# Performance work log

Measured on AMD Instinct MI355X. Metric: run time of the kernel, lower is better.

## Reference

```python
import jax, jax.numpy as jnp
import numpy as np

NUM_HEADS = 8
N_WIN = 7
TOPK = 4


def _grid2seq(x, rs, m):
    # x: (B, C, H, W) -> (B, m, nregion, reg_size, head_dim)
    B, C, H, W = x.shape
    rh, rw = H // rs[0], W // rs[1]
    d = C // m
    x = x.reshape(B, m, d, rh, rs[0], rw, rs[1])
    x = jnp.einsum('bmdhpwq->bmhwpqd', x).reshape(B, m, rh * rw, rs[0] * rs[1], d)
    return x, rh, rw


def _seq2grid(x, rh, rw, rs):
    B, m, nreg, rsq, d = x.shape
    x = x.reshape(B, m, rh, rw, rs[0], rs[1], d)
    return jnp.einsum('bmhwpqd->bmdhpwq', x).reshape(B, m * d, rh * rs[0], rw * rs[1])


def setup_inputs() -> dict:
    key = jax.random.key(0)
    ks = jax.random.split(key, 7)
    C = 256
    inp = {
        'x': jax.random.normal(ks[0], (16, C, 56, 56), jnp.float32),
        'w_qkv': jax.random.normal(ks[1], (3 * C, C), jnp.float32) * 0.02,
        'b_qkv': jax.random.normal(ks[2], (3 * C,), jnp.float32) * 0.02,
        'w_lepe': jax.random.normal(ks[3], (C, 1, 3, 3), jnp.float32) * 0.02,
        'b_lepe': jax.random.normal(ks[4], (C,), jnp.float32) * 0.02,
        'w_out': jax.random.normal(ks[5], (C, C), jnp.float32) * 0.02,
        'b_out': jax.random.normal(ks[6], (C,), jnp.float32) * 0.02,
    }
    return inp


def reference(x, w_qkv, b_qkv, w_lepe, b_lepe, w_out, b_out):
    N, C, H, W = x.shape
    m = NUM_HEADS
    d = C // m
    scale = d ** (-0.5)
    rs = (max(1, H // N_WIN), max(1, W // N_WIN))  # (8, 8) here; H,W divisible -> no pad
    rh, rw = H // rs[0], W // rs[1]

    # 1x1 conv qkv projection
    qkv = jnp.einsum('nchw,oc->nohw', x, w_qkv) + b_qkv[None, :, None, None]
    q, k, v = jnp.split(qkv, 3, axis=1)

    # region-level routing (avg_pool over each region; exact divisibility -> plain mean)
    def region_mean(t):
        return t.reshape(N, C, rh, rs[0], rw, rs[1]).mean(axis=(3, 5))  # (N,C,rh,rw)

    q_r = jax.lax.stop_gradient(region_mean(q)).reshape(N, C, rh * rw).transpose(0, 2, 1)  # (N,nreg,C)
    k_r = jax.lax.stop_gradient(region_mean(k)).reshape(N, C, rh * rw)  # (N,C,nreg)
    a_r = q_r @ k_r  # (N, nreg, nreg)
    k_fixed = min(TOPK, a_r.shape[-1])
    _, idx_r = jax.lax.top_k(a_r, k_fixed)  # (N, nreg, topk)
    idx_r = jnp.broadcast_to(idx_r[:, None], (N, m, rh * rw, k_fixed))  # (N,m,nreg,topk)

    # token-level attention within routed regions
    q_seq, _, _ = _grid2seq(q, rs, m)  # (N,m,nreg,rs2,d)
    k_seq, _, _ = _grid2seq(k, rs, m)
    v_seq, _, _ = _grid2seq(v, rs, m)
    rs2 = k_seq.shape[-2]

    gather = jax.vmap(jax.vmap(lambda seq, i: seq[i]))  # over (batch, head)
    key_g = gather(k_seq, idx_r).reshape(N, m, rh * rw, k_fixed * rs2, d)
    val_g = gather(v_seq, idx_r).reshape(N, m, rh * rw, k_fixed * rs2, d)

    attn = jax.nn.softmax(jnp.einsum('bmnpd,bmnkd->bmnpk', q_seq * scale, key_g), axis=-1)
    out = jnp.einsum('bmnpk,bmnkd->bmnpd', attn, val_g)
    out = _seq2grid(out, rh, rw, rs)  # (N, C, H, W)

    # LEPE: depthwise 3x3 conv on v
    lepe = jax.lax.conv_general_dilated(
        v, w_lepe, window_strides=(1, 1), padding='SAME',
        feature_group_count=C, dimension_numbers=('NCHW', 'OIHW', 'NCHW'))
    out = out + lepe + b_lepe[None, :, None, None]

    # 1x1 conv output projection
    out = jnp.einsum('nchw,oc->nohw', out, w_out) + b_out[None, :, None, None]
    return out
```

## Files before the change

### kernel.cpp

```cpp
#include <hip/hip_runtime.h>
#include <cstdint>

#define DEV __device__ __forceinline__

using short8 = __attribute__((ext_vector_type(8))) short;
using f32x4  = __attribute__((ext_vector_type(4))) float;

#define MFMA __builtin_amdgcn_mfma_f32_16x16x32_bf16

DEV float bf2f(unsigned short u){
  union { unsigned int i; float f; } v; v.i = ((unsigned int)u) << 16; return v.f;
}
DEV unsigned short f2bf(float f){
  union { float f; unsigned int i; } v; v.f = f;
  unsigned int x = v.i;
  return (unsigned short)((x + 0x7fffu + ((x >> 16) & 1u)) >> 16);
}
DEV unsigned int cvtpk(float a, float b){
  unsigned int r;
  asm("v_cvt_pk_bf16_f32 %0, %1, %2" : "=v"(r) : "v"(a), "v"(b));
  return r;
}

__global__ __launch_bounds__(256) void k_prep(const float* __restrict__ w_qkv,
                                              const float* __restrict__ w_out,
                                              unsigned short* __restrict__ wqh_t,
                                              unsigned short* __restrict__ woh_t,
                                              unsigned short* __restrict__ wol_t){
  int i = blockIdx.x*256 + threadIdx.x;
  if (i < 196608){
    int o = i >> 8, c = i & 255, kc = c >> 5, kk = c & 31;
    wqh_t[kc*24576 + o*32 + kk] = f2bf(w_qkv[i]);
  } else {
    int j = i - 196608;
    if (j < 65536){
      int o = j >> 8, c = j & 255, kc = c >> 5, kk = c & 31;
      float v = w_out[j];
      unsigned short h = f2bf(v);
      int dst = kc*8192 + o*32 + kk;
      woh_t[dst] = h;
      wol_t[dst] = f2bf(v - bf2f(h));
    }
  }
}

__global__ __launch_bounds__(256) void k_qrkr(const float* __restrict__ xbar,
                                              const float* __restrict__ w_qkv,
                                              const float* __restrict__ b_qkv,
                                              float* __restrict__ q_r,
                                              float* __restrict__ k_r){
  __shared__ float4 xb4[448];
  const int wb = blockIdx.x, n = blockIdx.y, rz = blockIdx.z, t = threadIdx.x;
  {
    const float4* src = (const float4*)(xbar + (size_t)n*12544) + rz*448;
    for (int i = t; i < 448; i += 256) xb4[i] = src[i];
  }
  const int wrow = wb*64 + (t>>2), kl = t&3;
  float4 wreg[16];
  {
    const float4* wsrc = (const float4*)(w_qkv + (size_t)wrow*256) + kl*16;
    #pragma unroll
    for (int i = 0; i < 16; ++i) wreg[i] = wsrc[i];
  }
  __syncthreads();
  const float bias = b_qkv[wrow];
  for (int rl = 0; rl < 7; ++rl){
    float s = 0.f;
    #pragma unroll
    for (int i = 0; i < 16; ++i){
      float4 a = wreg[i], b = xb4[rl*64 + kl*16 + i];
      s += a.x*b.x + a.y*b.y + a.z*b.z + a.w*b.w;
    }
    s += __shfl_xor(s, 1, 64);
    s += __shfl_xor(s, 2, 64);
    if (kl == 0){
      int reg = rz*7 + rl;
      if (wrow < 256) q_r[((size_t)n*49 + reg)*256 + wrow] = s + bias;
      else            k_r[((size_t)n*49 + reg)*256 + wrow - 256] = s + bias;
    }
  }
}

__global__ __launch_bounds__(64) void k_topk(const float* __restrict__ q_r,
                                             const float* __restrict__ k_r,
                                             int* __restrict__ idx){
  __shared__ float sc[49];
  const int qreg = blockIdx.x, n = blockIdx.y, l = threadIdx.x;
  const float* qrow = q_r + ((size_t)n*49 + qreg)*256;
  const float q0 = qrow[l], q1 = qrow[l+64], q2 = qrow[l+128], q3 = qrow[l+192];
  for (int kr = 0; kr < 49; ++kr){
    const float* krow = k_r + ((size_t)n*49 + kr)*256;
    float s = q0*krow[l] + q1*krow[l+64] + q2*krow[l+128] + q3*krow[l+192];
    #pragma unroll
    for (int m = 1; m < 64; m <<= 1) s += __shfl_xor(s, m, 64);
    if (l == 0) sc[kr] = s;
  }
  __syncthreads();
  if (l == 0){
    #pragma unroll
    for (int s = 0; s < 4; ++s){
      float best = -3.4e38f; int bi = 0;
      for (int kr = 0; kr < 49; ++kr) if (sc[kr] > best){ best = sc[kr]; bi = kr; }
      idx[((size_t)n*49 + qreg)*4 + s] = bi;
      sc[bi] = -3.4e38f;
    }
  }
}

__global__ __launch_bounds__(256) void k_qkv(const float* __restrict__ x,
                                             const unsigned short* __restrict__ wqh_t,
                                             const float* __restrict__ b_qkv,
                                             unsigned short* __restrict__ q_rm,
                                             unsigned short* __restrict__ k_rm,
                                             unsigned short* __restrict__ v_t,
                                             float* __restrict__ xbar){
  __shared__ unsigned short xl[64*256];
  const int lin = blockIdx.x;
  const int xcd = lin & 7, jj = lin >> 3;
  const int jobid = xcd*294 + jj;
  const int z = jobid % 3;
  const int pair = jobid / 3;
  const int reg = pair % 49, n = pair / 49;

  const int ry = reg/7, rx = reg%7;
  const int t = threadIdx.x, w = t>>6, g = (t>>4)&3, c16 = t&15;
  {
    const int pq = (t & 15)*4, cc = t >> 4;
    const int row = pq >> 3, col = pq & 7;
    const float* src = x + ((size_t)n*256 + cc)*3136 + (ry*8 + row)*56 + rx*8 + col;
    float rs[16];
    #pragma unroll
    for (int ci = 0; ci < 16; ++ci){
      float4 v4 = *reinterpret_cast<const float4*>(src + (size_t)ci*16*3136);
      int c = ci*16 + cc;
      xl[((pq+0)*256 + c) ^ (((pq+0)&15)<<3)] = f2bf(v4.x);
      xl[((pq+1)*256 + c) ^ (((pq+1)&15)<<3)] = f2bf(v4.y);
      xl[((pq+2)*256 + c) ^ (((pq+2)&15)<<3)] = f2bf(v4.z);
      xl[((pq+3)*256 + c) ^ (((pq+3)&15)<<3)] = f2bf(v4.w);
      rs[ci] = v4.x + v4.y + v4.z + v4.w;
    }
    if (z == 0){
      #pragma unroll
      for (int ci = 0; ci < 16; ++ci){
        float r = rs[ci];
        r += __shfl_xor(r, 1, 64);
        r += __shfl_xor(r, 2, 64);
        r += __shfl_xor(r, 4, 64);
        r += __shfl_xor(r, 8, 64);
        if ((t & 15) == 0)
          xbar[((size_t)n*49 + reg)*256 + ci*16 + (t>>4)] = r * (1.0f/64.0f);
      }
    }
  }
  __syncthreads();
  const size_t rb = (size_t)(n*8)*49 + reg;
  const int osw = w*16;

  if (z < 2){
    f32x4 acc[4][4] = {};
    for (int kc = 0; kc < 8; ++kc){
      short8 xf[4];
      #pragma unroll
      for (int pt = 0; pt < 4; ++pt){
        int p = pt*16 + c16;
        xf[pt] = *reinterpret_cast<const short8*>(&xl[(p*256 + kc*32 + 8*g) ^ ((p&15)<<3)]);
      }
      #pragma unroll
      for (int oi = 0; oi < 4; ++oi){
        const int os = z*256 + oi*64 + osw;
        short8 wf = *reinterpret_cast<const short8*>(wqh_t + (size_t)kc*24576 + (os + c16)*32 + 8*g);
        #pragma unroll
        for (int pt = 0; pt < 4; ++pt)
          acc[oi][pt] = MFMA(xf[pt], wf, acc[oi][pt], 0, 0, 0);
      }
    }
    #pragma unroll
    for (int oi = 0; oi < 4; ++oi){
      const int o = z*256 + oi*64 + osw + c16;
      const float bias = b_qkv[o];
      const int oc = o & 255, hh = oc >> 5, dd = oc & 31;
      unsigned short* dst = ((z == 0) ? q_rm : k_rm) + (rb + hh*49)*2048 + dd;
      #pragma unroll
      for (int pt = 0; pt < 4; ++pt)
        #pragma unroll
        for (int r = 0; r < 4; ++r){
          int tok = pt*16 + 4*g + r;
          dst[tok*32] = f2bf(acc[oi][pt][r] + bias);
        }
    }
  } else {
    f32x4 acc[4][4] = {};
    for (int kc = 0; kc < 8; ++kc){
      short8 xf[4];
      #pragma unroll
      for (int pt = 0; pt < 4; ++pt){
        int p = pt*16 + c16;
        xf[pt] = *reinterpret_cast<const short8*>(&xl[(p*256 + kc*32 + 8*g) ^ ((p&15)<<3)]);
      }
      #pragma unroll
      for (int oi = 0; oi < 4; ++oi){
        const int os = oi*64 + osw;
        short8 wf = *reinterpret_cast<const short8*>(wqh_t + (size_t)kc*24576 + (512 + os + c16)*32 + 8*g);
        #pragma unroll
        for (int pt = 0; pt < 4; ++pt)
          acc[oi][pt] = MFMA(wf, xf[pt], acc[oi][pt], 0, 0, 0);
      }
    }
    #pragma unroll
    for (int oi = 0; oi < 4; ++oi){
      #pragma unroll
      for (int r = 0; r < 4; ++r){
        int c = oi*64 + osw + 4*g + r;
        const float bias = b_qkv[512 + c];
        int hh = c >> 5, ch = c & 31;
        unsigned short* dst = v_t + (rb + hh*49)*2048 + ch*32;
        #pragma unroll
        for (int pt = 0; pt < 4; ++pt){
          int tok = pt*16 + c16;
          dst[(tok>>5)*1024 + (tok&31)] = f2bf(acc[oi][pt][r] + bias);
        }
      }
    }
  }
}

__global__ __launch_bounds__(256, 4) void k_attn(const unsigned short* __restrict__ q_rm,
                                                 const unsigned short* __restrict__ k_rm,
                                                 const unsigned short* __restrict__ v_t,
                                                 const int* __restrict__ idx,
                                                 const float* __restrict__ w_lepe,
                                                 const float* __restrict__ b_lepe,
                                                 unsigned short* __restrict__ att_hi,
                                                 unsigned short* __restrict__ att_lo){
  __shared__ unsigned short halo[10*320];
  __shared__ float wl_s[288];
  __shared__ float bl_s[32];

  const int lin = blockIdx.x + 49*(blockIdx.y + 8*blockIdx.z);
  const int xcd = lin & 7, j = lin >> 3;
  const int jq = j / 49;
  const int qreg = j - jq*49;
  const int hn = jq*8 + xcd;
  const int h = hn & 7, n = hn >> 3;

  const int t = threadIdx.x, w = t>>6, g = (t>>4)&3, c16 = t&15;
  const int ry = qreg/7, rx = qreg%7;
  const int gy0 = ry*8;

  int4 ridx = *reinterpret_cast<const int4*>(idx + ((size_t)n*49 + qreg)*4);
  int regs[4] = {ridx.x, ridx.y, ridx.z, ridx.w};

  const size_t hb = ((size_t)(n*8 + h))*49;

  wl_s[t < 288 ? t : 0] = w_lepe[h*288 + (t < 288 ? t : 0)];
  if (t < 32){
    wl_s[256 + t] = w_lepe[h*288 + 256 + t];
    bl_s[t] = b_lepe[h*32 + t];
  }
  #pragma unroll
  for (int pass = 0; pass < 2; ++pass){
    int s = pass ? (256 + t) : t;
    if (pass == 0 || t < 64){
      const int dy = s >> 5, c = s & 31;
      const int yy = gy0 + dy - 1;
      short8 inner = {0,0,0,0,0,0,0,0};
      unsigned short eL = 0, eR = 0;
      if (yy >= 0 && yy < 56){
        const int iry = yy >> 3, y7 = yy & 7;
        const size_t rowb = (size_t)(y7>>2)*1024 + c*32 + (y7&3)*8;
        inner = *reinterpret_cast<const short8*>(v_t + (hb + iry*7 + rx)*2048 + rowb);
        if (rx > 0) eL = v_t[(hb + iry*7 + rx - 1)*2048 + rowb + 7];
        if (rx < 6) eR = v_t[(hb + iry*7 + rx + 1)*2048 + rowb];
      }
      unsigned short* drow = &halo[dy*320 + c*10];
      drow[0] = eL;
      #pragma unroll
      for (int jj2 = 0; jj2 < 8; ++jj2) drow[1 + jj2] = (unsigned short)inner[jj2];
      drow[9] = eR;
    }
  }

  const int qtok = w*16 + c16;
  short8 qf = *reinterpret_cast<const short8*>(q_rm + (hb + qreg)*2048 + qtok*32 + 8*g);

  const float scale2 = 0.1767766952966369f * 1.4426950408889634f;
  const int srcA = (t & 15) | ((t & 16) << 1);
  const int srcB = srcA + 16;
  const bool gsel = (t & 32) != 0;

  float m_run = -3.4e38f, su = 0.f;
  f32x4 oacc[2] = {};

  #pragma unroll
  for (int h2 = 0; h2 < 2; ++h2){
    f32x4 s[8];
    #pragma unroll
    for (int f = 0; f < 8; ++f){
      const int tt = (f&3)*16 + c16;
      short8 kf = *reinterpret_cast<const short8*>(
          k_rm + (hb + regs[h2*2 + (f>>2)])*2048 + tt*32 + 8*g);
      f32x4 z = {0.f, 0.f, 0.f, 0.f};
      s[f] = MFMA(kf, qf, z, 0, 0, 0);
    }

    float ml = -3.4e38f;
    #pragma unroll
    for (int f = 0; f < 8; ++f)
      #pragma unroll
      for (int r = 0; r < 4; ++r) ml = fmaxf(ml, s[f][r]);
    ml = fmaxf(ml, __shfl_xor(ml, 16, 64));
    ml = fmaxf(ml, __shfl_xor(ml, 32, 64));

    const float mnew = (h2 == 0) ? ml : fmaxf(m_run, ml);
    if (h2 != 0){
      const float resc = exp2f((m_run - mnew) * scale2);
      su *= resc;
      float rq[4];
      #pragma unroll
      for (int r = 0; r < 4; ++r)
        rq[r] = __shfl(resc, 4*g + r, 64);
      #pragma unroll
      for (int dt = 0; dt < 2; ++dt)
        #pragma unroll
        for (int r = 0; r < 4; ++r)
          oacc[dt][r] *= rq[r];
    }
    m_run = mnew;

    const float nms = -mnew * scale2;
    #pragma unroll
    for (int f = 0; f < 8; ++f)
      #pragma unroll
      for (int r = 0; r < 4; ++r){
        float e = exp2f(fmaf(s[f][r], scale2, nms));
        s[f][r] = e; su += e;
      }

    #pragma unroll
    for (int tcl = 0; tcl < 4; ++tcl){
      const int fb = (tcl>>1)*4 + (tcl&1)*2;
      unsigned int a0 = cvtpk(s[fb][0],   s[fb][1]);
      unsigned int a1 = cvtpk(s[fb][2],   s[fb][3]);
      unsigned int b0 = cvtpk(s[fb+1][0], s[fb+1][1]);
      unsigned int b1 = cvtpk(s[fb+1][2], s[fb+1][3]);
      unsigned int wa0 = __shfl((int)a0, srcA, 64), wa1 = __shfl((int)a1, srcA, 64);
      unsigned int wa2 = __shfl((int)a0, srcB, 64), wa3 = __shfl((int)a1, srcB, 64);
      unsigned int wb0 = __shfl((int)b0, srcA, 64), wb1 = __shfl((int)b1, srcA, 64);
      unsigned int wb2 = __shfl((int)b0, srcB, 64), wb3 = __shfl((int)b1, srcB, 64);
      union { unsigned int u[4]; short8 s8; } pfu;
      pfu.u[0] = gsel ? wb0 : wa0;
      pfu.u[1] = gsel ? wb1 : wa1;
      pfu.u[2] = gsel ? wb2 : wa2;
      pfu.u[3] = gsel ? wb3 : wa3;
      const size_t vb = (hb + regs[h2*2 + (tcl>>1)])*2048 + (tcl&1)*1024 + 8*g;
      #pragma unroll
      for (int dt = 0; dt < 2; ++dt){
        short8 vf = *reinterpret_cast<const short8*>(v_t + vb + (dt*16 + c16)*32);
        oacc[dt] = MFMA(pfu.s8, vf, oacc[dt], 0, 0, 0);
      }
    }
  }

  su += __shfl_xor(su, 16, 64);
  su += __shfl_xor(su, 32, 64);
  const float inv_lane = __builtin_amdgcn_rcpf(su);
  float invq[4];
  #pragma unroll
  for (int r = 0; r < 4; ++r)
    invq[r] = __shfl(inv_lane, 4*g + r, 64);

  __syncthreads();
  const int tok0 = w*16 + 4*g;
  const int ty = tok0>>3, tx0 = tok0&7;
  #pragma unroll
  for (int dt = 0; dt < 2; ++dt){
    const int cl = dt*16 + c16;
    float wl[9];
    #pragma unroll
    for (int kk = 0; kk < 9; ++kk) wl[kk] = wl_s[cl*9 + kk];
    const float bl = bl_s[cl];
    float vwin[3][6];
    #pragma unroll
    for (int dy = 0; dy < 3; ++dy){
      const unsigned short* hrow = &halo[(ty+dy)*320 + cl*10 + tx0];
      #pragma unroll
      for (int jj = 0; jj < 6; ++jj)
        vwin[dy][jj] = bf2f(hrow[jj]);
    }
    #pragma unroll
    for (int r = 0; r < 4; ++r){
      float a = fmaf(oacc[dt][r], invq[r], bl);
      #pragma unroll
      for (int dy = 0; dy < 3; ++dy)
        #pragma unroll
        for (int dx = 0; dx < 3; ++dx)
          a += wl[dy*3 + dx] * vwin[dy][r + dx];
      int tok = tok0 + r;
      size_t o = ((size_t)(n*49 + qreg)*8 + h)*2048 + tok*32 + dt*16 + c16;
      unsigned short hi = (unsigned short)cvtpk(a, a);
      att_hi[o] = hi;
      float alo = a - bf2f(hi);
      att_lo[o] = (unsigned short)cvtpk(alo, alo);
    }
  }
}

__global__ __launch_bounds__(512) void k_oproj(const unsigned short* __restrict__ ah_,
                                               const unsigned short* __restrict__ al_,
                                               const unsigned short* __restrict__ wh_t,
                                               const unsigned short* __restrict__ wl_t,
                                               const float* __restrict__ b_out,
                                               float* __restrict__ out){
  const int lin = blockIdx.x;
  const int jobid = (lin & 7)*98 + (lin >> 3);
  const int reg = jobid % 49, n = jobid / 49;
  const int t = threadIdx.x, w8 = t>>6, g = (t>>4)&3, c16 = t&15;
  const int ry = reg/7, rx = reg%7;
  const size_t abase = ((size_t)(n*49 + reg))*8*2048;
  const int os1 = w8*16, os2 = os1 + 128;
  f32x4 acc[2][4] = {};
  for (int kc = 0; kc < 8; ++kc){
    const size_t wb = (size_t)kc*8192 + 8*g;
    short8 wh1 = *reinterpret_cast<const short8*>(wh_t + wb + (os1 + c16)*32);
    short8 wl1 = *reinterpret_cast<const short8*>(wl_t + wb + (os1 + c16)*32);
    short8 wh2 = *reinterpret_cast<const short8*>(wh_t + wb + (os2 + c16)*32);
    short8 wl2 = *reinterpret_cast<const short8*>(wl_t + wb + (os2 + c16)*32);
    #pragma unroll
    for (int pt = 0; pt < 4; ++pt){
      size_t off = abase + (size_t)kc*2048 + (pt*16 + c16)*32 + 8*g;
      short8 xh = *reinterpret_cast<const short8*>(ah_ + off);
      short8 xl = *reinterpret_cast<const short8*>(al_ + off);
      acc[0][pt] = MFMA(wh1, xh, acc[0][pt], 0, 0, 0);
      acc[0][pt] = MFMA(wh1, xl, acc[0][pt], 0, 0, 0);
      acc[0][pt] = MFMA(wl1, xh, acc[0][pt], 0, 0, 0);
      acc[1][pt] = MFMA(wh2, xh, acc[1][pt], 0, 0, 0);
      acc[1][pt] = MFMA(wh2, xl, acc[1][pt], 0, 0, 0);
      acc[1][pt] = MFMA(wl2, xh, acc[1][pt], 0, 0, 0);
    }
  }
  #pragma unroll
  for (int s = 0; s < 2; ++s){
    const int os = s ? os2 : os1;
    #pragma unroll
    for (int r = 0; r < 4; ++r){
      int o = os + 4*g + r;
      float bias = b_out[o];
      #pragma unroll
      for (int pt = 0; pt < 4; ++pt){
        int tok = pt*16 + c16;
        int p = (ry*8 + (tok>>3))*56 + rx*8 + (tok&7);
        out[((size_t)n*256 + o)*3136 + p] = acc[s][pt][r] + bias;
      }
    }
  }
}

extern "C" void kernel_launch(void* const* d_in, const int* in_sizes, int n_in,
                              void* d_out, int out_size, void* d_ws, size_t ws_size,
                              hipStream_t stream){
  const float* x      = (const float*)d_in[0];
  const float* w_qkv  = (const float*)d_in[1];
  const float* b_qkv  = (const float*)d_in[2];
  const float* w_lepe = (const float*)d_in[3];
  const float* b_lepe = (const float*)d_in[4];
  const float* w_out  = (const float*)d_in[5];
  const float* b_out  = (const float*)d_in[6];
  float* out = (float*)d_out;

  char* ws = (char*)d_ws;
  size_t off = 0;
  auto take = [&](size_t bytes)->char*{
    char* p = ws + off; off += (bytes + 255) & ~(size_t)255; return p;
  };
  const size_t TEN = (size_t)16*3136*256*2;
  unsigned short* q_rm   = (unsigned short*)take(TEN);
  unsigned short* k_rm   = (unsigned short*)take(TEN);
  unsigned short* v_t    = (unsigned short*)take(TEN);
  unsigned short* att_hi = (unsigned short*)take(TEN);
  unsigned short* att_lo = (unsigned short*)take(TEN);
  float* xbar = (float*)take((size_t)16*49*256*4);
  float* q_r  = (float*)take((size_t)16*49*256*4);
  float* k_r  = (float*)take((size_t)16*49*256*4);
  int*   idxb = (int*)take((size_t)16*49*4*4);
  unsigned short* wqh_t = (unsigned short*)take((size_t)768*256*2);
  unsigned short* woh_t = (unsigned short*)take((size_t)256*256*2);
  unsigned short* wol_t = (unsigned short*)take((size_t)256*256*2);

  k_prep <<<dim3(1024), 256, 0, stream>>>(w_qkv, w_out, wqh_t, woh_t, wol_t);
  k_qkv  <<<dim3(2352), 256, 0, stream>>>(x, wqh_t, b_qkv, q_rm, k_rm, v_t, xbar);
  k_qrkr <<<dim3(8, 16, 7), 256, 0, stream>>>(xbar, w_qkv, b_qkv, q_r, k_r);
  k_topk <<<dim3(49, 16), 64, 0, stream>>>(q_r, k_r, idxb);
  k_attn <<<dim3(49, 8, 16), 256, 0, stream>>>(q_rm, k_rm, v_t, idxb, w_lepe, b_lepe, att_hi, att_lo);
  k_oproj<<<dim3(784), 512, 0, stream>>>(att_hi, att_lo, woh_t, wol_t, b_out, out);
}
```

Measured before the change: 236.6 us.

## Split x transpose into separate kernel and widen qkv GEMM blocks

Result: slower. 251.8 us (+6.4%).

```diff
diff --git a/kernel.cpp b/kernel.cpp
--- a/kernel.cpp
+++ b/kernel.cpp
@@ -44,6 +44,52 @@
   }
 }
 
+__global__ __launch_bounds__(256) void k_xt(const float* __restrict__ x,
+                                            unsigned short* __restrict__ xt,
+                                            float* __restrict__ xbar){
+  __shared__ unsigned short xl[64*256];
+  const int lin = blockIdx.x;
+  const int jobid = (lin & 7)*98 + (lin >> 3);
+  const int reg = jobid % 49, n = jobid / 49;
+  const int ry = reg/7, rx = reg%7;
+  const int t = threadIdx.x;
+  {
+    const int pq = (t & 15)*4, cc = t >> 4;
+    const int row = pq >> 3, col = pq & 7;
+    const float* src = x + ((size_t)n*256 + cc)*3136 + (ry*8 + row)*56 + rx*8 + col;
+    float rs[16];
+    #pragma unroll
+    for (int ci = 0; ci < 16; ++ci){
+      float4 v4 = *reinterpret_cast<const float4*>(src + (size_t)ci*16*3136);
+      int c = ci*16 + cc;
+      xl[((pq+0)*256 + c) ^ (((pq+0)&15)<<3)] = f2bf(v4.x);
+      xl[((pq+1)*256 + c) ^ (((pq+1)&15)<<3)] = f2bf(v4.y);
+      xl[((pq+2)*256 + c) ^ (((pq+2)&15)<<3)] = f2bf(v4.z);
+      xl[((pq+3)*256 + c) ^ (((pq+3)&15)<<3)] = f2bf(v4.w);
+      rs[ci] = v4.x + v4.y + v4.z + v4.w;
+    }
+    #pragma unroll
+    for (int ci = 0; ci < 16; ++ci){
+      float r = rs[ci];
+      r += __shfl_xor(r, 1, 64);
+      r += __shfl_xor(r, 2, 64);
+      r += __shfl_xor(r, 4, 64);
+      r += __shfl_xor(r, 8, 64);
+      if ((t & 15) == 0)
+        xbar[((size_t)n*49 + reg)*256 + ci*16 + (t>>4)] = r * (1.0f/64.0f);
+    }
+  }
+  __syncthreads();
+  unsigned short* dst = xt + (size_t)(n*49 + reg)*16384;
+  const int tok = t >> 2, cg = (t & 3)*8;
+  #pragma unroll
+  for (int kc = 0; kc < 8; ++kc){
+    short8 v = *reinterpret_cast<const short8*>(
+        &xl[(tok*256 + kc*32 + cg) ^ ((tok&15)<<3)]);
+    *reinterpret_cast<short8*>(dst + kc*2048 + tok*32 + cg) = v;
+  }
+}
+
 __global__ __launch_bounds__(256) void k_qrkr(const float* __restrict__ xbar,
                                               const float* __restrict__ w_qkv,
                                               const float* __restrict__ b_qkv,
@@ -107,14 +153,12 @@
   }
 }
 
-__global__ __launch_bounds__(256) void k_qkv(const float* __restrict__ x,
+__global__ __launch_bounds__(512) void k_qkv(const unsigned short* __restrict__ xt,
                                              const unsigned short* __restrict__ wqh_t,
                                              const float* __restrict__ b_qkv,
                                              unsigned short* __restrict__ q_rm,
                                              unsigned short* __restrict__ k_rm,
-                                             unsigned short* __restrict__ v_t,
-                                             float* __restrict__ xbar){
-  __shared__ unsigned short xl[64*256];
+                                             unsigned short* __restrict__ v_t){
   const int lin = blockIdx.x;
   const int xcd = lin & 7, jj = lin >> 3;
   const int jobid = xcd*294 + jj;
@@ -122,61 +166,26 @@
   const int pair = jobid / 3;
   const int reg = pair % 49, n = pair / 49;
 
-  const int ry = reg/7, rx = reg%7;
-  const int t = threadIdx.x, w = t>>6, g = (t>>4)&3, c16 = t&15;
-  {
-    const int pq = (t & 15)*4, cc = t >> 4;
-    const int row = pq >> 3, col = pq & 7;
-    const float* src = x + ((size_t)n*256 + cc)*3136 + (ry*8 + row)*56 + rx*8 + col;
-    float rs[16];
-    #pragma unroll
-    for (int ci = 0; ci < 16; ++ci){
-      float4 v4 = *reinterpret_cast<const float4*>(src + (size_t)ci*16*3136);
-      int c = ci*16 + cc;
-      xl[((pq+0)*256 + c) ^ (((pq+0)&15)<<3)] = f2bf(v4.x);
-      xl[((pq+1)*256 + c) ^ (((pq+1)&15)<<3)] = f2bf(v4.y);
-      xl[((pq+2)*256 + c) ^ (((pq+2)&15)<<3)] = f2bf(v4.z);
-      xl[((pq+3)*256 + c) ^ (((pq+3)&15)<<3)] = f2bf(v4.w);
-      rs[ci] = v4.x + v4.y + v4.z + v4.w;
-    }
-    if (z == 0){
-      #pragma unroll
-      for (int ci = 0; ci < 16; ++ci){
-        float r = rs[ci];
-        r += __shfl_xor(r, 1, 64);
-        r += __shfl_xor(r, 2, 64);
-        r += __shfl_xor(r, 4, 64);
-        r += __shfl_xor(r, 8, 64);
-        if ((t & 15) == 0)
-          xbar[((size_t)n*49 + reg)*256 + ci*16 + (t>>4)] = r * (1.0f/64.0f);
-      }
-    }
-  }
-  __syncthreads();
+  const int t = threadIdx.x, w8 = t>>6, g = (t>>4)&3, c16 = t&15;
+  const unsigned short* xb = xt + (size_t)(n*49 + reg)*16384;
   const size_t rb = (size_t)(n*8)*49 + reg;
-  const int osw = w*16;
-
+  const int os1 = w8*16, os2 = os1 + 128;
+
+  f32x4 acc[2][4] = {};
   if (z < 2){
-    f32x4 acc[4][4] = {};
     for (int kc = 0; kc < 8; ++kc){
-      short8 xf[4];
+      short8 wf1 = *reinterpret_cast<const short8*>(wqh_t + (size_t)kc*24576 + (z*256 + os1 + c16)*32 + 8*g);
+      short8 wf2 = *reinterpret_cast<const short8*>(wqh_t + (size_t)kc*24576 + (z*256 + os2 + c16)*32 + 8*g);
       #pragma unroll
       for (int pt = 0; pt < 4; ++pt){
-        int p = pt*16 + c16;
-        xf[pt] = *reinterpret_cast<const short8*>(&xl[(p*256 + kc*32 + 8*g) ^ ((p&15)<<3)]);
-      }
-      #pragma unroll
-      for (int oi = 0; oi < 4; ++oi){
-        const int os = z*256 + oi*64 + osw;
-        short8 wf = *reinterpret_cast<const short8*>(wqh_t + (size_t)kc*24576 + (os + c16)*32 + 8*g);
-        #pragma unroll
-        for (int pt = 0; pt < 4; ++pt)
-          acc[oi][pt] = MFMA(xf[pt], wf, acc[oi][pt], 0, 0, 0);
-      }
-    }
-    #pragma unroll
-    for (int oi = 0; oi < 4; ++oi){
-      const int o = z*256 + oi*64 + osw + c16;
+        short8 xf = *reinterpret_cast<const short8*>(xb + kc*2048 + (pt*16 + c16)*32 + 8*g);
+        acc[0][pt] = MFMA(xf, wf1, acc[0][pt], 0, 0, 0);
+        acc[1][pt] = MFMA(xf, wf2, acc[1][pt], 0, 0, 0);
+      }
+    }
+    #pragma unroll
+    for (int s = 0; s < 2; ++s){
+      const int o = z*256 + (s ? os2 : os1) + c16;
       const float bias = b_qkv[o];
       const int oc = o & 255, hh = oc >> 5, dd = oc & 31;
       unsigned short* dst = ((z == 0) ? q_rm : k_rm) + (rb + hh*49)*2048 + dd;
@@ -185,39 +194,32 @@
         #pragma unroll
         for (int r = 0; r < 4; ++r){
           int tok = pt*16 + 4*g + r;
-          dst[tok*32] = f2bf(acc[oi][pt][r] + bias);
+          dst[tok*32] = f2bf(acc[s][pt][r] + bias);
         }
     }
   } else {
-    f32x4 acc[4][4] = {};
     for (int kc = 0; kc < 8; ++kc){
-      short8 xf[4];
+      short8 wf1 = *reinterpret_cast<const short8*>(wqh_t + (size_t)kc*24576 + (512 + os1 + c16)*32 + 8*g);
+      short8 wf2 = *reinterpret_cast<const short8*>(wqh_t + (size_t)kc*24576 + (512 + os2 + c16)*32 + 8*g);
       #pragma unroll
       for (int pt = 0; pt < 4; ++pt){
-        int p = pt*16 + c16;
-        xf[pt] = *reinterpret_cast<const short8*>(&xl[(p*256 + kc*32 + 8*g) ^ ((p&15)<<3)]);
-      }
-      #pragma unroll
-      for (int oi = 0; oi < 4; ++oi){
-        const int os = oi*64 + osw;
-        short8 wf = *reinterpret_cast<const short8*>(wqh_t + (size_t)kc*24576 + (512 + os + c16)*32 + 8*g);
-        #pragma unroll
-        for (int pt = 0; pt < 4; ++pt)
-          acc[oi][pt] = MFMA(wf, xf[pt], acc[oi][pt], 0, 0, 0);
-      }
-    }
-    #pragma unroll
-    for (int oi = 0; oi < 4; ++oi){
+        short8 xf = *reinterpret_cast<const short8*>(xb + kc*2048 + (pt*16 + c16)*32 + 8*g);
+        acc[0][pt] = MFMA(wf1, xf, acc[0][pt], 0, 0, 0);
+        acc[1][pt] = MFMA(wf2, xf, acc[1][pt], 0, 0, 0);
+      }
+    }
+    #pragma unroll
+    for (int s = 0; s < 2; ++s){
       #pragma unroll
       for (int r = 0; r < 4; ++r){
-        int c = oi*64 + osw + 4*g + r;
+        int c = (s ? os2 : os1) + 4*g + r;
         const float bias = b_qkv[512 + c];
         int hh = c >> 5, ch = c & 31;
         unsigned short* dst = v_t + (rb + hh*49)*2048 + ch*32;
         #pragma unroll
         for (int pt = 0; pt < 4; ++pt){
           int tok = pt*16 + c16;
-          dst[(tok>>5)*1024 + (tok&31)] = f2bf(acc[oi][pt][r] + bias);
+          dst[(tok>>5)*1024 + (tok&31)] = f2bf(acc[s][pt][r] + bias);
         }
       }
     }
@@ -473,6 +475,7 @@
     char* p = ws + off; off += (bytes + 255) & ~(size_t)255; return p;
   };
   const size_t TEN = (size_t)16*3136*256*2;
+  unsigned short* xt     = (unsigned short*)take(TEN);
   unsigned short* q_rm   = (unsigned short*)take(TEN);
   unsigned short* k_rm   = (unsigned short*)take(TEN);
   unsigned short* v_t    = (unsigned short*)take(TEN);
@@ -487,7 +490,8 @@
   unsigned short* wol_t = (unsigned short*)take((size_t)256*256*2);
 
   k_prep <<<dim3(1024), 256, 0, stream>>>(w_qkv, w_out, wqh_t, woh_t, wol_t);
-  k_qkv  <<<dim3(2352), 256, 0, stream>>>(x, wqh_t, b_qkv, q_rm, k_rm, v_t, xbar);
+  k_xt   <<<dim3(784), 256, 0, stream>>>(x, xt, xbar);
+  k_qkv  <<<dim3(2352), 512, 0, stream>>>(xt, wqh_t, b_qkv, q_rm, k_rm, v_t);
   k_qrkr <<<dim3(8, 16, 7), 256, 0, stream>>>(xbar, w_qkv, b_qkv, q_r, k_r);
   k_topk <<<dim3(49, 16), 64, 0, stream>>>(q_r, k_r, idxb);
   k_attn <<<dim3(49, 8, 16), 256, 0, stream>>>(q_rm, k_rm, v_t, idxb, w_lepe, b_lepe, att_hi, att_lo);
```
